# Kernel tuning notes

Measured on AMD Instinct MI355X. Metric: run time of the kernel, lower is better.

Reference implementation:

```python
import jax, jax.numpy as jnp
import numpy as np

VOCAB = 65
N_EMBD = 32
BLOCK = 8
N_HEADS = 4
HEAD = N_EMBD // N_HEADS  # 8
SQRT_C = float(N_EMBD) ** 0.5  # faithful bug: scores are MULTIPLIED by sqrt(n_embd)


def setup_inputs() -> dict:
    key = jax.random.key(0)
    ks = jax.random.split(key, 12)
    B, T = 65536, 8
    idx = jax.random.randint(ks[0], (B, T), 0, VOCAB, dtype=jnp.int64 if jax.config.jax_enable_x64 else jnp.int32)
    targets = jax.random.randint(ks[1], (B, T), 0, VOCAB, dtype=idx.dtype)
    s = 1.0 / np.sqrt(N_EMBD)
    return {
        "idx": idx,
        "targets": targets,
        "tok_emb": jax.random.normal(ks[2], (VOCAB, N_EMBD), jnp.float32),
        "pos_emb": jax.random.normal(ks[3], (BLOCK, N_EMBD), jnp.float32),
        # per-head Q/K/V projections stacked: [n_heads, n_embd, head_size]
        "Wq": jax.random.normal(ks[4], (N_HEADS, N_EMBD, HEAD), jnp.float32) * s,
        "Wk": jax.random.normal(ks[5], (N_HEADS, N_EMBD, HEAD), jnp.float32) * s,
        "Wv": jax.random.normal(ks[6], (N_HEADS, N_EMBD, HEAD), jnp.float32) * s,
        "W_mlp": jax.random.normal(ks[7], (N_EMBD, N_EMBD), jnp.float32) * s,
        "b_mlp": jnp.zeros((N_EMBD,), jnp.float32),
        "W_lm": jax.random.normal(ks[8], (N_EMBD, VOCAB), jnp.float32) * s,
        "b_lm": jnp.zeros((VOCAB,), jnp.float32),
    }


def reference(idx, targets, tok_emb, pos_emb, Wq, Wk, Wv, W_mlp, b_mlp, W_lm, b_lm):
    B, T = idx.shape
    x = tok_emb[idx] + pos_emb[:T]                       # [B,T,C]
    q = jnp.einsum('btc,hcd->bhtd', x, Wq)               # [B,H,T,D]
    k = jnp.einsum('btc,hcd->bhtd', x, Wk)
    v = jnp.einsum('btc,hcd->bhtd', x, Wv)
    wei = jnp.einsum('bhtd,bhsd->bhts', q, k) * SQRT_C   # faithful: * C**0.5
    tril = jnp.tril(jnp.ones((T, T), bool))
    wei = jnp.where(tril, wei, -jnp.inf)
    wei = jax.nn.softmax(wei, axis=-1)
    out = jnp.einsum('bhts,bhsd->bhtd', wei, v)          # [B,H,T,D]
    x = out.transpose(0, 2, 1, 3).reshape(B, T, N_EMBD)  # concat heads
    x = jax.nn.relu(x @ W_mlp + b_mlp)                   # MLP
    logits = x @ W_lm + b_lm                             # [B,T,V]
    logits = logits.reshape(B * T, VOCAB)
    logp = jax.nn.log_softmax(logits, axis=-1)
    tgt = targets.reshape(B * T)
    loss = -jnp.take_along_axis(logp, tgt[:, None], axis=-1).mean()
    return logits, loss
```

## Files before the change

### kernel.cpp

```cpp
#include <hip/hip_runtime.h>
#include <hip/hip_bf16.h>

#define VOCAB   65
#define SQRT_C  5.656854249492381f
#define BATCHES 65536
#define ROWS    (BATCHES * 8)
#define TABSZ   (8 * VOCAB * 32)
#define PAIRS   (BATCHES / 2)
#define NBLOCKS 2048
#define NWAVES  (NBLOCKS * 4)

typedef __attribute__((ext_vector_type(8))) short  short8;
typedef __attribute__((ext_vector_type(4))) float  float4v;

__device__ __forceinline__ void wave_fence() {
    __asm__ volatile("s_waitcnt lgkmcnt(0)" ::: "memory");
}
__device__ __forceinline__ short bfbits(float f) {
    __hip_bfloat16 h = __float2bfloat16(f);
    return *reinterpret_cast<short*>(&h);
}

__global__ void qkv_table_kernel(const float* __restrict__ tok_emb,
                                 const float* __restrict__ pos_emb,
                                 const float* __restrict__ Wq,
                                 const float* __restrict__ Wk,
                                 const float* __restrict__ Wv,
                                 float* __restrict__ qtab,
                                 float* __restrict__ ktab,
                                 float* __restrict__ vtab,
                                 float* __restrict__ loss_acc,
                                 unsigned* __restrict__ done_ctr) {
    int o = blockIdx.x * 256 + threadIdx.x;
    if (o == 0) { loss_acc[0] = 0.f; done_ctr[0] = 0u; }
    if (o >= 3 * TABSZ) return;
    int table = o / TABSZ;
    int r = o - table * TABSZ;
    int pair = r >> 5;
    int cd = r & 31;
    int t = pair / VOCAB;
    int tok = pair - t * VOCAB;
    int h = cd >> 3, d = cd & 7;
    const float* W = (table == 0) ? Wq : (table == 1) ? Wk : Wv;
    float acc = 0.f;
    #pragma unroll
    for (int c = 0; c < 32; ++c) {
        float xc = tok_emb[tok * 32 + c] + pos_emb[t * 32 + c];
        acc += xc * W[h * 256 + c * 8 + d];
    }
    if (table == 0) acc *= SQRT_C;
    float* tab = (table == 0) ? qtab : (table == 1) ? ktab : vtab;
    tab[r] = acc;
}

#define GATHER(TOKV)                                                         \
  { int c1 = l + 64;                                                         \
    int s0_ = (l >> 1) & 7,  g0 = l >> 4,  d20 = l & 1;                      \
    int s1_ = (c1 >> 1) & 7, g1 = c1 >> 4, d21 = c1 & 1;                     \
    int ts0 = __shfl((TOKV), (g0 & 1) * 8 + s0_);                            \
    int ts1 = __shfl((TOKV), (g1 & 1) * 8 + s1_);                            \
    int ga0 = (s0_ * VOCAB + ts0) * 32 + (g0 >> 1) * 8 + d20 * 4;            \
    int ga1 = (s1_ * VOCAB + ts1) * 32 + (g1 >> 1) * 8 + d21 * 4;            \
    kr0 = *(const float4*)(ktab + ga0); kr1 = *(const float4*)(ktab + ga1);  \
    vr0 = *(const float4*)(vtab + ga0); vr1 = *(const float4*)(vtab + ga1);  \
    int tt = __shfl((TOKV), b2 * 8 + t);                                     \
    const float* qp_ = qtab + (t * VOCAB + tt) * 32 + h * 8;                 \
    qf0 = *(const float4*)(qp_); qf1 = *(const float4*)(qp_ + 4); }

__global__ __launch_bounds__(256) void fused_kernel(
        const int* __restrict__ idx, const int* __restrict__ targets,
        const float* __restrict__ qtab, const float* __restrict__ ktab,
        const float* __restrict__ vtab,
        const float* __restrict__ W_mlp,
        const float* __restrict__ b_mlp,
        const float* __restrict__ W_lm,
        const float* __restrict__ b_lm,
        float* __restrict__ out_logits,
        float* __restrict__ loss_acc,
        unsigned* __restrict__ done_ctr,
        float* __restrict__ out_loss) {
    __shared__ __align__(16) float sK[4][544];
    __shared__ __align__(16) float sV[4][544];
    __shared__ __align__(16) unsigned short sX3[4][640];
    __shared__ float wsum[4];

    const int tid = threadIdx.x;
    const int w = tid >> 6, l = tid & 63;
    const int q4 = l >> 4;
    const int n  = l & 15;
    const int t  = l & 7, b2 = (l >> 3) & 1, h = q4;

    const int la0 = (l >> 4) * 68 + ((l >> 1) & 7) * 8 + (l & 1) * 4;
    const int la1 = ((l + 64) >> 4) * 68 + ((l >> 1) & 7) * 8 + (l & 1) * 4;

    short8 wmf[2], wlf[4], wlf4;
    #pragma unroll
    for (int c = 0; c < 2; ++c)
        #pragma unroll
        for (int j = 0; j < 8; ++j)
            wmf[c][j] = bfbits(W_mlp[(q4 * 8 + j) * 32 + c * 16 + n]);
    #pragma unroll
    for (int c = 0; c < 4; ++c)
        #pragma unroll
        for (int j = 0; j < 8; ++j)
            wlf[c][j] = bfbits(W_lm[(q4 * 8 + j) * VOCAB + c * 16 + n]);
    #pragma unroll
    for (int j = 0; j < 8; ++j)
        wlf4[j] = (n == 0) ? bfbits(W_lm[(q4 * 8 + j) * VOCAB + 64]) : (short)0;
    float bmc[2], blc[4];
    #pragma unroll
    for (int c = 0; c < 2; ++c) bmc[c] = b_mlp[c * 16 + n];
    #pragma unroll
    for (int c = 0; c < 4; ++c) blc[c] = b_lm[c * 16 + n];
    const float bl64 = b_lm[64];
    const float4v zf = {0.f, 0.f, 0.f, 0.f};

    float loss_local = 0.f;

    int pb = blockIdx.x * 4 + w;
    int tokv = 0, tgv = 0;
    if (l < 16) { tokv = idx[pb * 16 + l]; tgv = targets[pb * 16 + l]; }
    float4 kr0, kr1, vr0, vr1, qf0, qf1;
    GATHER(tokv)

    for (; pb < PAIRS; pb += NWAVES) {
        *(float4*)(&sK[w][la0]) = kr0;  *(float4*)(&sK[w][la1]) = kr1;
        *(float4*)(&sV[w][la0]) = vr0;  *(float4*)(&sV[w][la1]) = vr1;
        wave_fence();

        const int pbn = pb + NWAVES;
        int tokv_n = 0, tgv_n = 0;
        if (pbn < PAIRS && l < 16) {
            tokv_n = idx[pbn * 16 + l];
            tgv_n  = targets[pbn * 16 + l];
        }
        int tgrc[4];
        #pragma unroll
        for (int i = 0; i < 4; ++i) tgrc[i] = __shfl(tgv, q4 * 4 + i);

        const float* kb = &sK[w][(h * 2 + b2) * 68];
        const float* vb = &sV[w][(h * 2 + b2) * 68];
        float sc[8], m = -1e30f;
        #pragma unroll
        for (int s = 0; s < 8; ++s) {
            float4 k0 = *(const float4*)(kb + s * 8);
            float4 k1 = *(const float4*)(kb + s * 8 + 4);
            float d = qf0.x * k0.x + qf0.y * k0.y + qf0.z * k0.z + qf0.w * k0.w
                    + qf1.x * k1.x + qf1.y * k1.y + qf1.z * k1.z + qf1.w * k1.w;
            sc[s] = d;
            if (s <= t) m = fmaxf(m, d);
        }
        float p[8], sum = 0.f;
        #pragma unroll
        for (int s = 0; s < 8; ++s) {
            p[s] = (s <= t) ? __expf(sc[s] - m) : 0.f;
            sum += p[s];
        }
        float inv = 1.f / sum;
        float o[8];
        #pragma unroll
        for (int d = 0; d < 8; ++d) o[d] = 0.f;
        #pragma unroll
        for (int s = 0; s < 8; ++s) {
            float4 v0 = *(const float4*)(vb + s * 8);
            float4 v1 = *(const float4*)(vb + s * 8 + 4);
            o[0] += p[s] * v0.x; o[1] += p[s] * v0.y;
            o[2] += p[s] * v0.z; o[3] += p[s] * v0.w;
            o[4] += p[s] * v1.x; o[5] += p[s] * v1.y;
            o[6] += p[s] * v1.z; o[7] += p[s] * v1.w;
        }
        short8 a2;
        #pragma unroll
        for (int d = 0; d < 8; ++d) a2[d] = bfbits(o[d] * inv);

        if (pbn < PAIRS) { GATHER(tokv_n) }

        float4v d0 = __builtin_amdgcn_mfma_f32_16x16x32_bf16(a2, wmf[0], zf, 0, 0, 0);
        float4v d1 = __builtin_amdgcn_mfma_f32_16x16x32_bf16(a2, wmf[1], zf, 0, 0, 0);
        #pragma unroll
        for (int i = 0; i < 4; ++i) {
            int row = q4 * 4 + i;
            sX3[w][row * 40 + n]      = (unsigned short)bfbits(fmaxf(d0[i] + bmc[0], 0.f));
            sX3[w][row * 40 + 16 + n] = (unsigned short)bfbits(fmaxf(d1[i] + bmc[1], 0.f));
        }
        wave_fence();
        short8 a3 = *(const short8*)(&sX3[w][n * 40 + q4 * 8]);

        float4v Lc[4];
        #pragma unroll
        for (int c = 0; c < 4; ++c)
            Lc[c] = __builtin_amdgcn_mfma_f32_16x16x32_bf16(a3, wlf[c], zf, 0, 0, 0);
        float4v L64 = __builtin_amdgcn_mfma_f32_16x16x32_bf16(a3, wlf4, zf, 0, 0, 0);

        size_t rb = (size_t)pb * 16;
        float part[4] = {0.f, 0.f, 0.f, 0.f};
        #pragma unroll
        for (int c = 0; c < 4; ++c) {
            #pragma unroll
            for (int i = 0; i < 4; ++i) {
                float Lv = Lc[c][i] + blc[c];
                out_logits[(rb + q4 * 4 + i) * VOCAB + c * 16 + n] = Lv;
                part[i] += __expf(Lv);
                if (c * 16 + n == tgrc[i]) loss_local -= Lv;
            }
        }
        if (n == 0) {
            #pragma unroll
            for (int i = 0; i < 4; ++i) {
                float Lv = L64[i] + bl64;
                out_logits[(rb + q4 * 4 + i) * VOCAB + 64] = Lv;
                part[i] += __expf(Lv);
                if (tgrc[i] == 64) loss_local -= Lv;
            }
        }
        #pragma unroll
        for (int off = 1; off < 16; off <<= 1) {
            #pragma unroll
            for (int i = 0; i < 4; ++i) part[i] += __shfl_xor(part[i], off);
        }
        if (n == 0)
            loss_local += __logf(part[0]) + __logf(part[1])
                        + __logf(part[2]) + __logf(part[3]);

        tokv = tokv_n; tgv = tgv_n;
    }

    #pragma unroll
    for (int off = 1; off < 64; off <<= 1) loss_local += __shfl_xor(loss_local, off);
    if (l == 0) wsum[w] = loss_local;
    __syncthreads();
    if (tid == 0) {
        atomicAdd(loss_acc, wsum[0] + wsum[1] + wsum[2] + wsum[3]);
        __threadfence();
        unsigned done = atomicAdd(done_ctr, 1u);
        if (done == NBLOCKS - 1) {
            __threadfence();
            float tot = atomicAdd(loss_acc, 0.f);
            out_loss[0] = tot * (1.f / (float)ROWS);
        }
    }
}

extern "C" void kernel_launch(void* const* d_in, const int* in_sizes, int n_in,
                              void* d_out, int out_size, void* d_ws, size_t ws_size,
                              hipStream_t stream) {
    const int* idx        = (const int*)d_in[0];
    const int* targets    = (const int*)d_in[1];
    const float* tok_emb  = (const float*)d_in[2];
    const float* pos_emb  = (const float*)d_in[3];
    const float* Wq       = (const float*)d_in[4];
    const float* Wk       = (const float*)d_in[5];
    const float* Wv       = (const float*)d_in[6];
    const float* W_mlp    = (const float*)d_in[7];
    const float* b_mlp    = (const float*)d_in[8];
    const float* W_lm     = (const float*)d_in[9];
    const float* b_lm     = (const float*)d_in[10];
    float* out            = (float*)d_out;

    float* ws        = (float*)d_ws;
    float* loss_ptr  = ws;
    unsigned* ctr    = (unsigned*)(ws + 1);
    float* qtab      = ws + 16;
    float* ktab      = qtab + TABSZ;
    float* vtab      = ktab + TABSZ;
    float* out_loss  = out + (size_t)ROWS * VOCAB;

    qkv_table_kernel<<<(3 * TABSZ + 255) / 256, 256, 0, stream>>>(
        tok_emb, pos_emb, Wq, Wk, Wv, qtab, ktab, vtab, loss_ptr, ctr);

    fused_kernel<<<NBLOCKS, 256, 0, stream>>>(
        idx, targets, qtab, ktab, vtab, W_mlp, b_mlp, W_lm, b_lm,
        out, loss_ptr, ctr, out_loss);
}
```

Before: 350.3 us.

## Replace persistent grid-stride loop with one-pair-per-wave grid and prepacked weight fragments

The persistent 2048-block kernel with its software-pipelined gather loop is replaced by a grid of PAIRS/4 blocks, where each wave handles exactly one batch pair. The MFMA weight fragments for W_mlp and W_lm are now converted to bf16 once in the table kernel, so each wave loads them with a few vector loads instead of many scalar gathers plus conversions. The single global loss atomic is spread across 16 padded slots, and the kernel gets a launch-bounds occupancy hint of 7. The trade-off is about 8192 blocks each paying per-block setup and an end-of-block atomic, and losing the prefetch overlap of the next pair's gather.

Result: slower. 1.135 ms (+224.0%).

```diff
diff --git a/kernel.cpp b/kernel.cpp
--- a/kernel.cpp
+++ b/kernel.cpp
@@ -7,8 +7,8 @@
 #define ROWS    (BATCHES * 8)
 #define TABSZ   (8 * VOCAB * 32)
 #define PAIRS   (BATCHES / 2)
-#define NBLOCKS 2048
-#define NWAVES  (NBLOCKS * 4)
+#define NBLOCKS (PAIRS / 4)
+#define NFRAG   448
 
 typedef __attribute__((ext_vector_type(8))) short  short8;
 typedef __attribute__((ext_vector_type(4))) float  float4v;
@@ -26,57 +26,61 @@
                                  const float* __restrict__ Wq,
                                  const float* __restrict__ Wk,
                                  const float* __restrict__ Wv,
+                                 const float* __restrict__ W_mlp,
+                                 const float* __restrict__ W_lm,
                                  float* __restrict__ qtab,
                                  float* __restrict__ ktab,
                                  float* __restrict__ vtab,
-                                 float* __restrict__ loss_acc,
+                                 float* __restrict__ frag_tab,
+                                 float* __restrict__ loss_slots,
                                  unsigned* __restrict__ done_ctr) {
     int o = blockIdx.x * 256 + threadIdx.x;
-    if (o == 0) { loss_acc[0] = 0.f; done_ctr[0] = 0u; }
-    if (o >= 3 * TABSZ) return;
-    int table = o / TABSZ;
-    int r = o - table * TABSZ;
-    int pair = r >> 5;
-    int cd = r & 31;
-    int t = pair / VOCAB;
-    int tok = pair - t * VOCAB;
-    int h = cd >> 3, d = cd & 7;
-    const float* W = (table == 0) ? Wq : (table == 1) ? Wk : Wv;
-    float acc = 0.f;
-    #pragma unroll
-    for (int c = 0; c < 32; ++c) {
-        float xc = tok_emb[tok * 32 + c] + pos_emb[t * 32 + c];
-        acc += xc * W[h * 256 + c * 8 + d];
-    }
-    if (table == 0) acc *= SQRT_C;
-    float* tab = (table == 0) ? qtab : (table == 1) ? ktab : vtab;
-    tab[r] = acc;
-}
-
-#define GATHER(TOKV)                                                         \
-  { int c1 = l + 64;                                                         \
-    int s0_ = (l >> 1) & 7,  g0 = l >> 4,  d20 = l & 1;                      \
-    int s1_ = (c1 >> 1) & 7, g1 = c1 >> 4, d21 = c1 & 1;                     \
-    int ts0 = __shfl((TOKV), (g0 & 1) * 8 + s0_);                            \
-    int ts1 = __shfl((TOKV), (g1 & 1) * 8 + s1_);                            \
-    int ga0 = (s0_ * VOCAB + ts0) * 32 + (g0 >> 1) * 8 + d20 * 4;            \
-    int ga1 = (s1_ * VOCAB + ts1) * 32 + (g1 >> 1) * 8 + d21 * 4;            \
-    kr0 = *(const float4*)(ktab + ga0); kr1 = *(const float4*)(ktab + ga1);  \
-    vr0 = *(const float4*)(vtab + ga0); vr1 = *(const float4*)(vtab + ga1);  \
-    int tt = __shfl((TOKV), b2 * 8 + t);                                     \
-    const float* qp_ = qtab + (t * VOCAB + tt) * 32 + h * 8;                 \
-    qf0 = *(const float4*)(qp_); qf1 = *(const float4*)(qp_ + 4); }
-
-__global__ __launch_bounds__(256) void fused_kernel(
+    if (o < 16) loss_slots[o * 16] = 0.f;
+    if (o == 16) done_ctr[0] = 0u;
+
+    if (o < 3 * TABSZ) {
+        int table = o / TABSZ;
+        int r = o - table * TABSZ;
+        int pair = r >> 5;
+        int cd = r & 31;
+        int t = pair / VOCAB;
+        int tok = pair - t * VOCAB;
+        int h = cd >> 3, d = cd & 7;
+        const float* W = (table == 0) ? Wq : (table == 1) ? Wk : Wv;
+        float acc = 0.f;
+        #pragma unroll
+        for (int c = 0; c < 32; ++c) {
+            float xc = tok_emb[tok * 32 + c] + pos_emb[t * 32 + c];
+            acc += xc * W[h * 256 + c * 8 + d];
+        }
+        if (table == 0) acc *= SQRT_C;
+        float* tab = (table == 0) ? qtab : (table == 1) ? ktab : vtab;
+        tab[r] = acc;
+    } else if (o < 3 * TABSZ + NFRAG) {
+        int f = o - 3 * TABSZ;
+        int cls = f >> 6, lane = f & 63;
+        int q4l = lane >> 4, nl = lane & 15;
+        short8 v;
+        #pragma unroll
+        for (int j = 0; j < 8; ++j) {
+            int k = q4l * 8 + j;
+            if (cls < 2)       v[j] = bfbits(W_mlp[k * 32 + cls * 16 + nl]);
+            else if (cls < 6)  v[j] = bfbits(W_lm[k * VOCAB + (cls - 2) * 16 + nl]);
+            else               v[j] = (nl == 0) ? bfbits(W_lm[k * VOCAB + 64]) : (short)0;
+        }
+        ((short8*)frag_tab)[f] = v;
+    }
+}
+
+__global__ __launch_bounds__(256, 7) void fused_kernel(
         const int* __restrict__ idx, const int* __restrict__ targets,
         const float* __restrict__ qtab, const float* __restrict__ ktab,
         const float* __restrict__ vtab,
-        const float* __restrict__ W_mlp,
+        const float* __restrict__ frag_tab,
         const float* __restrict__ b_mlp,
-        const float* __restrict__ W_lm,
         const float* __restrict__ b_lm,
         float* __restrict__ out_logits,
-        float* __restrict__ loss_acc,
+        float* __restrict__ loss_slots,
         unsigned* __restrict__ done_ctr,
         float* __restrict__ out_loss) {
     __shared__ __align__(16) float sK[4][544];
@@ -90,23 +94,17 @@
     const int n  = l & 15;
     const int t  = l & 7, b2 = (l >> 3) & 1, h = q4;
 
-    const int la0 = (l >> 4) * 68 + ((l >> 1) & 7) * 8 + (l & 1) * 4;
-    const int la1 = ((l + 64) >> 4) * 68 + ((l >> 1) & 7) * 8 + (l & 1) * 4;
-
+    const int pb = blockIdx.x * 4 + w;
+
+    int tokv = 0, tgv = 0;
+    if (l < 16) { tokv = idx[pb * 16 + l]; tgv = targets[pb * 16 + l]; }
+
+    const short8* ftab = (const short8*)frag_tab;
     short8 wmf[2], wlf[4], wlf4;
-    #pragma unroll
-    for (int c = 0; c < 2; ++c)
-        #pragma unroll
-        for (int j = 0; j < 8; ++j)
-            wmf[c][j] = bfbits(W_mlp[(q4 * 8 + j) * 32 + c * 16 + n]);
-    #pragma unroll
-    for (int c = 0; c < 4; ++c)
-        #pragma unroll
-        for (int j = 0; j < 8; ++j)
-            wlf[c][j] = bfbits(W_lm[(q4 * 8 + j) * VOCAB + c * 16 + n]);
-    #pragma unroll
-    for (int j = 0; j < 8; ++j)
-        wlf4[j] = (n == 0) ? bfbits(W_lm[(q4 * 8 + j) * VOCAB + 64]) : (short)0;
+    wmf[0] = ftab[l];        wmf[1] = ftab[64 + l];
+    #pragma unroll
+    for (int c = 0; c < 4; ++c) wlf[c] = ftab[(2 + c) * 64 + l];
+    wlf4 = ftab[6 * 64 + l];
     float bmc[2], blc[4];
     #pragma unroll
     for (int c = 0; c < 2; ++c) bmc[c] = b_mlp[c * 16 + n];
@@ -115,127 +113,127 @@
     const float bl64 = b_lm[64];
     const float4v zf = {0.f, 0.f, 0.f, 0.f};
 
+    {
+        int c1 = l + 64;
+        int s0 = (l >> 1) & 7, g0 = l >> 4, d2 = l & 1, g1 = c1 >> 4;
+        int ts0 = __shfl(tokv, (g0 & 1) * 8 + s0);
+        int ts1 = __shfl(tokv, (g1 & 1) * 8 + s0);
+        int ga0 = (s0 * VOCAB + ts0) * 32 + (g0 >> 1) * 8 + d2 * 4;
+        int ga1 = (s0 * VOCAB + ts1) * 32 + (g1 >> 1) * 8 + d2 * 4;
+        int la0 = g0 * 68 + s0 * 8 + d2 * 4;
+        int la1 = g1 * 68 + s0 * 8 + d2 * 4;
+        *(float4*)(&sK[w][la0]) = *(const float4*)(ktab + ga0);
+        *(float4*)(&sK[w][la1]) = *(const float4*)(ktab + ga1);
+        *(float4*)(&sV[w][la0]) = *(const float4*)(vtab + ga0);
+        *(float4*)(&sV[w][la1]) = *(const float4*)(vtab + ga1);
+    }
+    const int tok_t = __shfl(tokv, b2 * 8 + t);
+    const float* qp = qtab + (t * VOCAB + tok_t) * 32 + h * 8;
+    const float4 q0 = *(const float4*)(qp);
+    const float4 q1 = *(const float4*)(qp + 4);
+    int tgrc[4];
+    #pragma unroll
+    for (int i = 0; i < 4; ++i) tgrc[i] = __shfl(tgv, q4 * 4 + i);
+    wave_fence();
+
+    const float* kb = &sK[w][(h * 2 + b2) * 68];
+    const float* vb = &sV[w][(h * 2 + b2) * 68];
+    float sc[8], m = -1e30f;
+    #pragma unroll
+    for (int s = 0; s < 8; ++s) {
+        float4 k0 = *(const float4*)(kb + s * 8);
+        float4 k1 = *(const float4*)(kb + s * 8 + 4);
+        float d = q0.x * k0.x + q0.y * k0.y + q0.z * k0.z + q0.w * k0.w
+                + q1.x * k1.x + q1.y * k1.y + q1.z * k1.z + q1.w * k1.w;
+        sc[s] = d;
+        if (s <= t) m = fmaxf(m, d);
+    }
+    float p[8], sum = 0.f;
+    #pragma unroll
+    for (int s = 0; s < 8; ++s) {
+        p[s] = (s <= t) ? __expf(sc[s] - m) : 0.f;
+        sum += p[s];
+    }
+    float inv = 1.f / sum;
+    float o[8];
+    #pragma unroll
+    for (int d = 0; d < 8; ++d) o[d] = 0.f;
+    #pragma unroll
+    for (int s = 0; s < 8; ++s) {
+        float4 v0 = *(const float4*)(vb + s * 8);
+        float4 v1 = *(const float4*)(vb + s * 8 + 4);
+        o[0] += p[s] * v0.x; o[1] += p[s] * v0.y;
+        o[2] += p[s] * v0.z; o[3] += p[s] * v0.w;
+        o[4] += p[s] * v1.x; o[5] += p[s] * v1.y;
+        o[6] += p[s] * v1.z; o[7] += p[s] * v1.w;
+    }
+    short8 a2;
+    #pragma unroll
+    for (int d = 0; d < 8; ++d) a2[d] = bfbits(o[d] * inv);
+
+    float4v d0 = __builtin_amdgcn_mfma_f32_16x16x32_bf16(a2, wmf[0], zf, 0, 0, 0);
+    float4v d1 = __builtin_amdgcn_mfma_f32_16x16x32_bf16(a2, wmf[1], zf, 0, 0, 0);
+    #pragma unroll
+    for (int i = 0; i < 4; ++i) {
+        int row = q4 * 4 + i;
+        sX3[w][row * 40 + n]      = (unsigned short)bfbits(fmaxf(d0[i] + bmc[0], 0.f));
+        sX3[w][row * 40 + 16 + n] = (unsigned short)bfbits(fmaxf(d1[i] + bmc[1], 0.f));
+    }
+    wave_fence();
+    short8 a3 = *(const short8*)(&sX3[w][n * 40 + q4 * 8]);
+
+    float4v Lc[4];
+    #pragma unroll
+    for (int c = 0; c < 4; ++c)
+        Lc[c] = __builtin_amdgcn_mfma_f32_16x16x32_bf16(a3, wlf[c], zf, 0, 0, 0);
+    float4v L64 = __builtin_amdgcn_mfma_f32_16x16x32_bf16(a3, wlf4, zf, 0, 0, 0);
+
     float loss_local = 0.f;
-
-    int pb = blockIdx.x * 4 + w;
-    int tokv = 0, tgv = 0;
-    if (l < 16) { tokv = idx[pb * 16 + l]; tgv = targets[pb * 16 + l]; }
-    float4 kr0, kr1, vr0, vr1, qf0, qf1;
-    GATHER(tokv)
-
-    for (; pb < PAIRS; pb += NWAVES) {
-        *(float4*)(&sK[w][la0]) = kr0;  *(float4*)(&sK[w][la1]) = kr1;
-        *(float4*)(&sV[w][la0]) = vr0;  *(float4*)(&sV[w][la1]) = vr1;
-        wave_fence();
-
-        const int pbn = pb + NWAVES;
-        int tokv_n = 0, tgv_n = 0;
-        if (pbn < PAIRS && l < 16) {
-            tokv_n = idx[pbn * 16 + l];
-            tgv_n  = targets[pbn * 16 + l];
-        }
-        int tgrc[4];
-        #pragma unroll
-        for (int i = 0; i < 4; ++i) tgrc[i] = __shfl(tgv, q4 * 4 + i);
-
-        const float* kb = &sK[w][(h * 2 + b2) * 68];
-        const float* vb = &sV[w][(h * 2 + b2) * 68];
-        float sc[8], m = -1e30f;
-        #pragma unroll
-        for (int s = 0; s < 8; ++s) {
-            float4 k0 = *(const float4*)(kb + s * 8);
-            float4 k1 = *(const float4*)(kb + s * 8 + 4);
-            float d = qf0.x * k0.x + qf0.y * k0.y + qf0.z * k0.z + qf0.w * k0.w
-                    + qf1.x * k1.x + qf1.y * k1.y + qf1.z * k1.z + qf1.w * k1.w;
-            sc[s] = d;
-            if (s <= t) m = fmaxf(m, d);
-        }
-        float p[8], sum = 0.f;
-        #pragma unroll
-        for (int s = 0; s < 8; ++s) {
-            p[s] = (s <= t) ? __expf(sc[s] - m) : 0.f;
-            sum += p[s];
-        }
-        float inv = 1.f / sum;
-        float o[8];
-        #pragma unroll
-        for (int d = 0; d < 8; ++d) o[d] = 0.f;
-        #pragma unroll
-        for (int s = 0; s < 8; ++s) {
-            float4 v0 = *(const float4*)(vb + s * 8);
-            float4 v1 = *(const float4*)(vb + s * 8 + 4);
-            o[0] += p[s] * v0.x; o[1] += p[s] * v0.y;
-            o[2] += p[s] * v0.z; o[3] += p[s] * v0.w;
-            o[4] += p[s] * v1.x; o[5] += p[s] * v1.y;
-            o[6] += p[s] * v1.z; o[7] += p[s] * v1.w;
-        }
-        short8 a2;
-        #pragma unroll
-        for (int d = 0; d < 8; ++d) a2[d] = bfbits(o[d] * inv);
-
-        if (pbn < PAIRS) { GATHER(tokv_n) }
-
-        float4v d0 = __builtin_amdgcn_mfma_f32_16x16x32_bf16(a2, wmf[0], zf, 0, 0, 0);
-        float4v d1 = __builtin_amdgcn_mfma_f32_16x16x32_bf16(a2, wmf[1], zf, 0, 0, 0);
+    size_t rb = (size_t)pb * 16;
+    float part[4] = {0.f, 0.f, 0.f, 0.f};
+    #pragma unroll
+    for (int c = 0; c < 4; ++c) {
         #pragma unroll
         for (int i = 0; i < 4; ++i) {
-            int row = q4 * 4 + i;
-            sX3[w][row * 40 + n]      = (unsigned short)bfbits(fmaxf(d0[i] + bmc[0], 0.f));
-            sX3[w][row * 40 + 16 + n] = (unsigned short)bfbits(fmaxf(d1[i] + bmc[1], 0.f));
-        }
-        wave_fence();
-        short8 a3 = *(const short8*)(&sX3[w][n * 40 + q4 * 8]);
-
-        float4v Lc[4];
-        #pragma unroll
-        for (int c = 0; c < 4; ++c)
-            Lc[c] = __builtin_amdgcn_mfma_f32_16x16x32_bf16(a3, wlf[c], zf, 0, 0, 0);
-        float4v L64 = __builtin_amdgcn_mfma_f32_16x16x32_bf16(a3, wlf4, zf, 0, 0, 0);
-
-        size_t rb = (size_t)pb * 16;
-        float part[4] = {0.f, 0.f, 0.f, 0.f};
-        #pragma unroll
-        for (int c = 0; c < 4; ++c) {
-            #pragma unroll
-            for (int i = 0; i < 4; ++i) {
-                float Lv = Lc[c][i] + blc[c];
-                out_logits[(rb + q4 * 4 + i) * VOCAB + c * 16 + n] = Lv;
-                part[i] += __expf(Lv);
-                if (c * 16 + n == tgrc[i]) loss_local -= Lv;
-            }
-        }
-        if (n == 0) {
-            #pragma unroll
-            for (int i = 0; i < 4; ++i) {
-                float Lv = L64[i] + bl64;
-                out_logits[(rb + q4 * 4 + i) * VOCAB + 64] = Lv;
-                part[i] += __expf(Lv);
-                if (tgrc[i] == 64) loss_local -= Lv;
-            }
-        }
-        #pragma unroll
-        for (int off = 1; off < 16; off <<= 1) {
-            #pragma unroll
-            for (int i = 0; i < 4; ++i) part[i] += __shfl_xor(part[i], off);
-        }
-        if (n == 0)
-            loss_local += __logf(part[0]) + __logf(part[1])
-                        + __logf(part[2]) + __logf(part[3]);
-
-        tokv = tokv_n; tgv = tgv_n;
-    }
+            float Lv = Lc[c][i] + blc[c];
+            out_logits[(rb + q4 * 4 + i) * VOCAB + c * 16 + n] = Lv;
+            part[i] += __expf(Lv);
+            if (c * 16 + n == tgrc[i]) loss_local -= Lv;
+        }
+    }
+    if (n == 0) {
+        #pragma unroll
+        for (int i = 0; i < 4; ++i) {
+            float Lv = L64[i] + bl64;
+            out_logits[(rb + q4 * 4 + i) * VOCAB + 64] = Lv;
+            part[i] += __expf(Lv);
+            if (tgrc[i] == 64) loss_local -= Lv;
+        }
+    }
+    #pragma unroll
+    for (int off = 1; off < 16; off <<= 1) {
+        #pragma unroll
+        for (int i = 0; i < 4; ++i) part[i] += __shfl_xor(part[i], off);
+    }
+    if (n == 0)
+        loss_local += __logf(part[0]) + __logf(part[1])
+                    + __logf(part[2]) + __logf(part[3]);
 
     #pragma unroll
     for (int off = 1; off < 64; off <<= 1) loss_local += __shfl_xor(loss_local, off);
     if (l == 0) wsum[w] = loss_local;
     __syncthreads();
     if (tid == 0) {
-        atomicAdd(loss_acc, wsum[0] + wsum[1] + wsum[2] + wsum[3]);
+        atomicAdd(&loss_slots[(blockIdx.x & 15) * 16],
+                  wsum[0] + wsum[1] + wsum[2] + wsum[3]);
         __threadfence();
         unsigned done = atomicAdd(done_ctr, 1u);
         if (done == NBLOCKS - 1) {
             __threadfence();
-            float tot = atomicAdd(loss_acc, 0.f);
+            float tot = 0.f;
+            #pragma unroll
+            for (int s = 0; s < 16; ++s)
+                tot += atomicAdd(&loss_slots[s * 16], 0.f);
             out_loss[0] = tot * (1.f / (float)ROWS);
         }
     }
@@ -257,18 +255,20 @@
     const float* b_lm     = (const float*)d_in[10];
     float* out            = (float*)d_out;
 
-    float* ws        = (float*)d_ws;
-    float* loss_ptr  = ws;
-    unsigned* ctr    = (unsigned*)(ws + 1);
-    float* qtab      = ws + 16;
-    float* ktab      = qtab + TABSZ;
-    float* vtab      = ktab + TABSZ;
-    float* out_loss  = out + (size_t)ROWS * VOCAB;
-
-    qkv_table_kernel<<<(3 * TABSZ + 255) / 256, 256, 0, stream>>>(
-        tok_emb, pos_emb, Wq, Wk, Wv, qtab, ktab, vtab, loss_ptr, ctr);
+    float* ws         = (float*)d_ws;
+    float* loss_slots = ws;
+    unsigned* ctr     = (unsigned*)(ws + 256);
+    float* frag       = ws + 272;
+    float* qtab       = ws + 272 + 1792;
+    float* ktab       = qtab + TABSZ;
+    float* vtab       = ktab + TABSZ;
+    float* out_loss   = out + (size_t)ROWS * VOCAB;
+
+    qkv_table_kernel<<<(3 * TABSZ + NFRAG + 255) / 256, 256, 0, stream>>>(
+        tok_emb, pos_emb, Wq, Wk, Wv, W_mlp, W_lm,
+        qtab, ktab, vtab, frag, loss_slots, ctr);
 
     fused_kernel<<<NBLOCKS, 256, 0, stream>>>(
-        idx, targets, qtab, ktab, vtab, W_mlp, b_mlp, W_lm, b_lm,
-        out, loss_ptr, ctr, out_loss);
-}
+        idx, targets, qtab, ktab, vtab, frag, b_mlp, b_lm,
+        out, loss_slots, ctr, out_loss);
+}
```
